# Performance work log

Hardware: AMD Instinct MI355X
Metric: run time of the kernel (lower is better)

Reference implementation:

```python
import jax, jax.numpy as jnp
import numpy as np

WEIGHT = 1000.0      # start/end cell penalty
LONELY_W = 15.0      # cell lit outside cluster
CLUSTER_W = 5.0      # cell unlit inside cluster
CELL_W = 20.0        # cell on a shortest manhattan path
CSIZE_W = 12.0       # cluster-size penalty
GAP_W = 300.0        # gap-to-endpoint penalty
H = W = 10


def _md(y1, x1, y2, x2):
    return jnp.abs(y1 - y2) + jnp.abs(x1 - x2)


def _per_sample(result, points):
    # result: [H, W] float, points: [2, 2] int (row, col) of start and end
    p0y, p0x = points[0, 0], points[0, 1]
    p1y, p1x = points[1, 0], points[1, 1]
    base = _md(p0y, p0x, p1y, p1x)

    loss_start = (2.0 - (result[p0y, p0x] + result[p1y, p1x])) * WEIGHT

    # 8-connected flood fill from start over cells whose value rounds to 1.
    mask = jnp.round(result) == 1.0
    seed = jnp.zeros((H, W), bool).at[p0y, p0x].set(True)

    def dilate(_, c):
        p = jnp.pad(c, 1)
        nb = (p[:-2, :-2] | p[:-2, 1:-1] | p[:-2, 2:] |
              p[1:-1, :-2] | p[1:-1, 2:] |
              p[2:, :-2] | p[2:, 1:-1] | p[2:, 2:])
        return c | (nb & mask)

    # 8-connected diameter of a 10x10 grid is 9; H+W iterations is a safe bound.
    cluster = jax.lax.fori_loop(0, H + W, dilate, seed)

    rows = jnp.arange(H)[:, None]
    cols = jnp.arange(W)[None, :]

    # per-cell manhattan detour penalty
    d2 = _md(rows, cols, p0y, p0x) + _md(rows, cols, p1y, p1x)
    delta = (d2 - base).astype(result.dtype)
    single_cell = jnp.sum(jnp.where(delta == 0.0,
                                    (1.0 - result) * CELL_W,
                                    result * delta * 0.5))

    # NB: the original tests [column, row] membership against [row, col]
    # cluster entries -> transposed membership map. Faithfully reproduced.
    in_cl = cluster.T
    csize = jnp.sum(cluster).astype(result.dtype)
    lonelyness = jnp.sum(jnp.where(in_cl, (1.0 - result) * CLUSTER_W,
                                   result * LONELY_W))
    cluster_size_pen = jnp.sum(jnp.where(in_cl, result * csize * CSIZE_W, 0.0))

    # nearest cluster cell to the end point (strict improvement over base)
    dist_end = _md(rows, cols, p1y, p1x)
    masked = jnp.where(cluster, dist_end, H * W + 10).reshape(-1)
    idx = jnp.argmin(masked)
    minval = masked[idx]
    better = minval < base
    ny = jnp.where(better, idx // W, p0y)
    nx = jnp.where(better, idx % W, p0x)
    gap = jnp.minimum(base, minval)

    oy = p1y - ny
    ox = p1x - nx

    def upd(cond, cy, cx, st):
        by, bx, bg = st
        d = _md(cy, cx, p1y, p1x)
        b = cond & (d < bg)
        return (jnp.where(b, cy, by), jnp.where(b, cx, bx), jnp.where(b, d, bg))

    st = (ny, nx, gap)
    c = ox < 0
    st = upd(c, ny, nx - 1, st)
    st = upd(c & (ny != 0), ny - 1, nx - 1, st)
    st = upd(c & (ny != H - 1), ny + 1, nx - 1, st)
    c = ox > 0
    st = upd(c, ny, nx + 1, st)
    st = upd(c & (ny != 0), ny - 1, nx + 1, st)
    st = upd(c & (ny != H - 1), ny + 1, nx + 1, st)
    st = upd(oy < 0, ny - 1, nx, st)
    st = upd(oy > 0, ny + 1, nx, st)
    ncy = jnp.clip(st[0], 0, H - 1)
    ncx = jnp.clip(st[1], 0, W - 1)

    gap_pen = gap.astype(result.dtype) * GAP_W * (1.0 - result[ncy, ncx])

    return loss_start + lonelyness + single_cell + cluster_size_pen + gap_pen


def setup_inputs() -> dict:
    key = jax.random.key(0)
    k1, k2 = jax.random.split(key)
    B = 262144
    result_given = jax.random.uniform(k1, (B, 1, H, W), dtype=jnp.float32)
    points_given = jax.random.randint(k2, (B, 2, 2), 0, 10, dtype=jnp.int64 if jax.config.jax_enable_x64 else jnp.int32)
    return {"result_given": result_given, "points_given": points_given}


def reference(result_given, points_given):
    losses = jax.vmap(_per_sample)(result_given[:, 0], points_given)
    return jnp.sum(losses).reshape(1)
```

## Files before the change

kernel.cpp:

```cpp
#include <hip/hip_runtime.h>
#include <cstdint>

#define GH 10
#define GW 10

__global__ __launch_bounds__(256, 1) void custom_loss_kernel(
    const float* __restrict__ result,
    const int* __restrict__ points,
    float* __restrict__ out,
    int B)
{
    const int t = blockIdx.x * blockDim.x + threadIdx.x;
    float loss = 0.f;
    if (t < B) {
        const float* __restrict__ r = result + (size_t)t * 100;
        const int4 p = ((const int4*)points)[t];
        const int p0y = p.x, p0x = p.y, p1y = p.z, p1x = p.w;
        const int dy0 = abs(p0y - p1y), dx0 = abs(p0x - p1x);
        const int base = dy0 + dx0;
        const int idx0 = p0y * GW + p0x;
        const int idx1 = p1y * GW + p1x;
        const float rs = r[idx0];
        const float re = r[idx1];

        float adxf[10], inboxf[10];
#pragma unroll
        for (int x = 0; x < 10; ++x) {
            const int a = abs(x - p0x) + abs(x - p1x) - dx0;
            adxf[x] = (float)a;
            inboxf[x] = (a == 0) ? 1.f : 0.f;
        }

        float sum_all = 0.f, sc = 0.f, boxSum = 0.f;
        uint64_t mlo = 0, mhi = 0;
#pragma unroll
        for (int y = 0; y < GH; ++y) {
            const float* rp = r + y * 10;
            const float4 a = *(const float4*)(rp);
            const float4 b = *(const float4*)(rp + 4);
            const float2 c = *(const float2*)(rp + 8);
            const float vv[10] = {a.x, a.y, a.z, a.w, b.x, b.y, b.z, b.w, c.x, c.y};
            const float rowacc = ((vv[0]+vv[1])+(vv[2]+vv[3])) +
                                 ((vv[4]+vv[5])+(vv[6]+vv[7])) + (vv[8]+vv[9]);
            sum_all += rowacc;
            const int ay = abs(y - p0y) + abs(y - p1y) - dy0;
            sc = fmaf((float)ay, rowacc, sc);
            float boxrow = 0.f;
            uint32_t rm = 0u;
#pragma unroll
            for (int x = 0; x < 10; ++x) {
                const float xv = vv[x];
                sc = fmaf(adxf[x], xv, sc);
                boxrow = fmaf(inboxf[x], xv, boxrow);
                rm |= (xv > 0.5f) ? (1u << x) : 0u;
            }
            boxSum += (ay == 0) ? boxrow : 0.f;
            if (y < 5) mlo |= (uint64_t)rm << (10 * y);
            else       mhi |= (uint64_t)rm << (10 * (y - 5));
        }

        const uint64_t M50 = (1ull << 50) - 1;
        const uint64_t C0  = 0x10040100401ull;
        const uint64_t NC0 = M50 & ~C0;
        const uint64_t NC9 = M50 & ~(C0 << 9);
        uint64_t clo = 0, chi = 0;
        if (idx0 < 50) clo = 1ull << idx0; else chi = 1ull << (idx0 - 50);
#pragma unroll 1
        for (int it = 0; it < GH + GW; ++it) {
            const uint64_t hlo = clo | ((clo << 1) & NC0) | ((clo >> 1) & NC9);
            const uint64_t hhi = chi | ((chi << 1) & NC0) | ((chi >> 1) & NC9);
            uint64_t nlo = (hlo | (hlo << 10) | (hlo >> 10) | ((hhi & 0x3FFull) << 40)) & mlo;
            uint64_t nhi = (hhi | (hhi << 10) | (hhi >> 10) | (hlo >> 40)) & mhi;
            nlo |= clo; nhi |= chi;
            if (nlo == clo && nhi == chi) break;
            clo = nlo; chi = nhi;
        }

        const int K = __popcll(clo) + __popcll(chi);

        float S_T = 0.f;
#pragma unroll
        for (int y = 0; y < GH; ++y) {
            const float* rp = r + y * 10;
            const float4 a = *(const float4*)(rp);
            const float4 b = *(const float4*)(rp + 4);
            const float2 c = *(const float2*)(rp + 8);
            const float vv[10] = {a.x, a.y, a.z, a.w, b.x, b.y, b.z, b.w, c.x, c.y};
#pragma unroll
            for (int x = 0; x < 10; ++x) {
                const int bpos = x * 10 + y;
                const uint32_t bit = (bpos < 50) ? (uint32_t)((clo >> bpos) & 1ull)
                                                 : (uint32_t)((chi >> (bpos - 50)) & 1ull);
                S_T = fmaf((float)bit, vv[x], S_T);
            }
        }

        int bestd = 1000, bidx = 0;
#pragma unroll
        for (int y = 0; y < GH; ++y) {
            const uint32_t rb = (uint32_t)((y < 5 ? (clo >> (10 * y))
                                                  : (chi >> (10 * (y - 5)))) & 0x3FFull);
            const uint32_t left  = rb & ((2u << p1x) - 1);
            const uint32_t right = rb >> p1x;
            const int dl = left  ? (p1x - (31 - __builtin_clz(left))) : 1000;
            const int dr = right ? __builtin_ctz(right) : 1000;
            int dx, xx;
            if (dl <= dr) { dx = dl; xx = p1x - dl; }
            else          { dx = dr; xx = p1x + dr; }
            const int d = abs(y - p1y) + dx;
            if (rb && d < bestd) { bestd = d; bidx = y * GW + xx; }
        }

        const bool better = bestd < base;
        const int ny = better ? bidx / 10 : p0y;
        const int nx = better ? bidx % 10 : p0x;
        const int gap = min(base, bestd);

        int by = ny, bx = nx, bg = gap;
        const int oy = p1y - ny, ox = p1x - nx;
        auto upd = [&](bool cond, int cy, int cx) {
            const int d = abs(cy - p1y) + abs(cx - p1x);
            if (cond && (d < bg)) { by = cy; bx = cx; bg = d; }
        };
        upd(ox < 0,                     ny,     nx - 1);
        upd((ox < 0) && (ny != 0),      ny - 1, nx - 1);
        upd((ox < 0) && (ny != GH - 1), ny + 1, nx - 1);
        upd(ox > 0,                     ny,     nx + 1);
        upd((ox > 0) && (ny != 0),      ny - 1, nx + 1);
        upd((ox > 0) && (ny != GH - 1), ny + 1, nx + 1);
        upd(oy < 0,                     ny - 1, nx);
        upd(oy > 0,                     ny + 1, nx);
        const int ncy = min(max(by, 0), GH - 1);
        const int ncx = min(max(bx, 0), GW - 1);
        const float rn = r[ncy * GW + ncx];

        const float csf = (float)K;
        const float nboxf = (float)((dy0 + 1) * (dx0 + 1));
        const float loss_start = (2.f - (rs + re)) * 1000.f;
        const float lon = 5.f * csf + 15.f * sum_all - 20.f * S_T;
        const float single_cell = 0.5f * sc + 20.f * (nboxf - boxSum);
        const float cpen = 12.f * csf * S_T;
        const float gap_pen = (float)gap * 300.f * (1.f - rn);
        loss = loss_start + lon + single_cell + cpen + gap_pen;
    }

#pragma unroll
    for (int off = 32; off > 0; off >>= 1)
        loss += __shfl_down(loss, off);
    __shared__ float wsum[4];
    const int lane = threadIdx.x & 63;
    const int wid = threadIdx.x >> 6;
    if (lane == 0) wsum[wid] = loss;
    __syncthreads();
    if (threadIdx.x == 0)
        atomicAdd(out, wsum[0] + wsum[1] + wsum[2] + wsum[3]);
}

extern "C" void kernel_launch(void* const* d_in, const int* in_sizes, int n_in,
                              void* d_out, int out_size, void* d_ws, size_t ws_size,
                              hipStream_t stream)
{
    const float* result = (const float*)d_in[0];
    const int* points   = (const int*)d_in[1];
    float* out = (float*)d_out;
    const int B = in_sizes[0] / 100;
    hipMemsetAsync(out, 0, sizeof(float), stream);
    const int block = 256;
    const int grid = (B + block - 1) / block;
    custom_loss_kernel<<<grid, block, 0, stream>>>(result, points, out, B);
}
```

Measured before the change: 182.6 us.

## Split each sample across two lanes, exchanging flood-fill halves via shuffles

Each sample is now handled by a pair of lanes, each owning five rows. Partial sums, the flood-fill bitmask halves and the nearest-cell search are combined with xor shuffles, and the launch bounds hint rises from 1 to 6 blocks. This doubles the thread count and cuts per-thread register use, aiming for more parallelism and better latency hiding on a memory-heavy kernel. The cost is a shuffle on every flood-fill iteration plus extra shuffles for the reductions, and the final scalar tail runs on only half the lanes.

```diff
diff --git a/kernel.cpp b/kernel.cpp
--- a/kernel.cpp
+++ b/kernel.cpp
@@ -4,17 +4,19 @@
 #define GH 10
 #define GW 10
 
-__global__ __launch_bounds__(256, 1) void custom_loss_kernel(
+__global__ __launch_bounds__(256, 6) void custom_loss_kernel(
     const float* __restrict__ result,
     const int* __restrict__ points,
     float* __restrict__ out,
     int B)
 {
-    const int t = blockIdx.x * blockDim.x + threadIdx.x;
+    const int tid = blockIdx.x * blockDim.x + threadIdx.x;
+    const int s = tid >> 1;
+    const int h = tid & 1;
     float loss = 0.f;
-    if (t < B) {
-        const float* __restrict__ r = result + (size_t)t * 100;
-        const int4 p = ((const int4*)points)[t];
+    if (s < B) {
+        const float* __restrict__ r = result + (size_t)s * 100;
+        const int4 p = ((const int4*)points)[s];
         const int p0y = p.x, p0x = p.y, p1y = p.z, p1x = p.w;
         const int dy0 = abs(p0y - p1y), dx0 = abs(p0x - p1x);
         const int base = dy0 + dx0;
@@ -23,83 +25,98 @@
         const float rs = r[idx0];
         const float re = r[idx1];
 
-        float adxf[10], inboxf[10];
+        float adxf[10];
+        uint32_t inbox_m = 0;
 #pragma unroll
         for (int x = 0; x < 10; ++x) {
             const int a = abs(x - p0x) + abs(x - p1x) - dx0;
             adxf[x] = (float)a;
-            inboxf[x] = (a == 0) ? 1.f : 0.f;
+            inbox_m |= (a == 0) ? (1u << x) : 0u;
         }
 
-        float sum_all = 0.f, sc = 0.f, boxSum = 0.f;
-        uint64_t mlo = 0, mhi = 0;
+        const int ybase = 5 * h;
+        const float* __restrict__ rh = r + ybase * 10;
+        float sum_h = 0.f, sc_h = 0.f, box_h = 0.f;
+        uint64_t mword = 0;
 #pragma unroll
-        for (int y = 0; y < GH; ++y) {
-            const float* rp = r + y * 10;
-            const float4 a = *(const float4*)(rp);
-            const float4 b = *(const float4*)(rp + 4);
-            const float2 c = *(const float2*)(rp + 8);
-            const float vv[10] = {a.x, a.y, a.z, a.w, b.x, b.y, b.z, b.w, c.x, c.y};
+        for (int i = 0; i < 5; ++i) {
+            const int y = ybase + i;
+            const float4 a4 = *(const float4*)(rh + i * 10);
+            const float4 b4 = *(const float4*)(rh + i * 10 + 4);
+            const float2 c2 = *(const float2*)(rh + i * 10 + 8);
+            const float vv[10] = {a4.x, a4.y, a4.z, a4.w,
+                                  b4.x, b4.y, b4.z, b4.w, c2.x, c2.y};
             const float rowacc = ((vv[0]+vv[1])+(vv[2]+vv[3])) +
                                  ((vv[4]+vv[5])+(vv[6]+vv[7])) + (vv[8]+vv[9]);
-            sum_all += rowacc;
+            sum_h += rowacc;
             const int ay = abs(y - p0y) + abs(y - p1y) - dy0;
-            sc = fmaf((float)ay, rowacc, sc);
+            sc_h = fmaf((float)ay, rowacc, sc_h);
             float boxrow = 0.f;
             uint32_t rm = 0u;
 #pragma unroll
             for (int x = 0; x < 10; ++x) {
                 const float xv = vv[x];
-                sc = fmaf(adxf[x], xv, sc);
-                boxrow = fmaf(inboxf[x], xv, boxrow);
+                sc_h = fmaf(adxf[x], xv, sc_h);
+                boxrow += ((inbox_m >> x) & 1u) ? xv : 0.f;
                 rm |= (xv > 0.5f) ? (1u << x) : 0u;
             }
-            boxSum += (ay == 0) ? boxrow : 0.f;
-            if (y < 5) mlo |= (uint64_t)rm << (10 * y);
-            else       mhi |= (uint64_t)rm << (10 * (y - 5));
+            box_h += (ay == 0) ? boxrow : 0.f;
+            mword |= (uint64_t)rm << (10 * i);
         }
+        const float sum_all = sum_h + __shfl_xor(sum_h, 1);
+        const float sc      = sc_h  + __shfl_xor(sc_h, 1);
+        const float boxSum  = box_h + __shfl_xor(box_h, 1);
 
         const uint64_t M50 = (1ull << 50) - 1;
         const uint64_t C0  = 0x10040100401ull;
         const uint64_t NC0 = M50 & ~C0;
         const uint64_t NC9 = M50 & ~(C0 << 9);
-        uint64_t clo = 0, chi = 0;
-        if (idx0 < 50) clo = 1ull << idx0; else chi = 1ull << (idx0 - 50);
+        uint64_t c = 0;
+        if (h == 0) { if (idx0 <  50) c = 1ull << idx0; }
+        else        { if (idx0 >= 50) c = 1ull << (idx0 - 50); }
 #pragma unroll 1
         for (int it = 0; it < GH + GW; ++it) {
-            const uint64_t hlo = clo | ((clo << 1) & NC0) | ((clo >> 1) & NC9);
-            const uint64_t hhi = chi | ((chi << 1) & NC0) | ((chi >> 1) & NC9);
-            uint64_t nlo = (hlo | (hlo << 10) | (hlo >> 10) | ((hhi & 0x3FFull) << 40)) & mlo;
-            uint64_t nhi = (hhi | (hhi << 10) | (hhi >> 10) | (hlo >> 40)) & mhi;
-            nlo |= clo; nhi |= chi;
-            if (nlo == clo && nhi == chi) break;
-            clo = nlo; chi = nhi;
+            const uint64_t ho = c | ((c << 1) & NC0) | ((c >> 1) & NC9);
+            const uint64_t hother =
+                (uint64_t)__shfl_xor((unsigned long long)ho, 1);
+            const uint64_t inc = h ? (hother >> 40) : ((hother & 0x3FFull) << 40);
+            const uint64_t n = ((ho | (ho << 10) | (ho >> 10) | inc) & mword) | c;
+            int ch = (n != c);
+            ch |= __shfl_xor(ch, 1);
+            c = n;
+            if (!ch) break;
         }
+        const int Kh = __popcll(c);
+        const int K = Kh + __shfl_xor(Kh, 1);
 
-        const int K = __popcll(clo) + __popcll(chi);
+        const uint64_t c_other = (uint64_t)__shfl_xor((unsigned long long)c, 1);
+        const uint64_t clo = h ? c_other : c;
+        const uint64_t chi = h ? c : c_other;
 
-        float S_T = 0.f;
+        const uint64_t wlo = clo >> (5 * h);
+        const uint64_t whi = chi >> (5 * h);
+        float st_h = 0.f;
 #pragma unroll
-        for (int y = 0; y < GH; ++y) {
-            const float* rp = r + y * 10;
-            const float4 a = *(const float4*)(rp);
-            const float4 b = *(const float4*)(rp + 4);
-            const float2 c = *(const float2*)(rp + 8);
-            const float vv[10] = {a.x, a.y, a.z, a.w, b.x, b.y, b.z, b.w, c.x, c.y};
+        for (int i = 0; i < 5; ++i) {
+            const float4 a4 = *(const float4*)(rh + i * 10);
+            const float4 b4 = *(const float4*)(rh + i * 10 + 4);
+            const float2 c2 = *(const float2*)(rh + i * 10 + 8);
+            const float vv[10] = {a4.x, a4.y, a4.z, a4.w,
+                                  b4.x, b4.y, b4.z, b4.w, c2.x, c2.y};
 #pragma unroll
             for (int x = 0; x < 10; ++x) {
-                const int bpos = x * 10 + y;
-                const uint32_t bit = (bpos < 50) ? (uint32_t)((clo >> bpos) & 1ull)
-                                                 : (uint32_t)((chi >> (bpos - 50)) & 1ull);
-                S_T = fmaf((float)bit, vv[x], S_T);
+                const uint64_t w = (x < 5) ? wlo : whi;
+                const uint32_t bit = (uint32_t)((w >> ((x % 5) * 10 + i)) & 1ull);
+                st_h = fmaf((float)bit, vv[x], st_h);
             }
         }
+        const float S_T = st_h + __shfl_xor(st_h, 1);
 
         int bestd = 1000, bidx = 0;
 #pragma unroll
-        for (int y = 0; y < GH; ++y) {
-            const uint32_t rb = (uint32_t)((y < 5 ? (clo >> (10 * y))
-                                                  : (chi >> (10 * (y - 5)))) & 0x3FFull);
+        for (int i = 0; i < 5; ++i) {
+            const int y = ybase + i;
+            const uint32_t rb = (uint32_t)((c >> (10 * i)) & 0x3FFull);
             const uint32_t left  = rb & ((2u << p1x) - 1);
             const uint32_t right = rb >> p1x;
             const int dl = left  ? (p1x - (31 - __builtin_clz(left))) : 1000;
@@ -110,38 +127,45 @@
             const int d = abs(y - p1y) + dx;
             if (rb && d < bestd) { bestd = d; bidx = y * GW + xx; }
         }
+        {
+            const int od = __shfl_xor(bestd, 1);
+            const int oi = __shfl_xor(bidx, 1);
+            if (od < bestd || (od == bestd && oi < bidx)) { bestd = od; bidx = oi; }
+        }
 
-        const bool better = bestd < base;
-        const int ny = better ? bidx / 10 : p0y;
-        const int nx = better ? bidx % 10 : p0x;
-        const int gap = min(base, bestd);
+        if (h == 0) {
+            const bool better = bestd < base;
+            const int ny = better ? bidx / 10 : p0y;
+            const int nx = better ? bidx % 10 : p0x;
+            const int gap = min(base, bestd);
 
-        int by = ny, bx = nx, bg = gap;
-        const int oy = p1y - ny, ox = p1x - nx;
-        auto upd = [&](bool cond, int cy, int cx) {
-            const int d = abs(cy - p1y) + abs(cx - p1x);
-            if (cond && (d < bg)) { by = cy; bx = cx; bg = d; }
-        };
-        upd(ox < 0,                     ny,     nx - 1);
-        upd((ox < 0) && (ny != 0),      ny - 1, nx - 1);
-        upd((ox < 0) && (ny != GH - 1), ny + 1, nx - 1);
-        upd(ox > 0,                     ny,     nx + 1);
-        upd((ox > 0) && (ny != 0),      ny - 1, nx + 1);
-        upd((ox > 0) && (ny != GH - 1), ny + 1, nx + 1);
-        upd(oy < 0,                     ny - 1, nx);
-        upd(oy > 0,                     ny + 1, nx);
-        const int ncy = min(max(by, 0), GH - 1);
-        const int ncx = min(max(bx, 0), GW - 1);
-        const float rn = r[ncy * GW + ncx];
+            int by = ny, bx = nx, bg = gap;
+            const int oy = p1y - ny, ox = p1x - nx;
+            auto upd = [&](bool cond, int cy, int cx) {
+                const int d = abs(cy - p1y) + abs(cx - p1x);
+                if (cond && (d < bg)) { by = cy; bx = cx; bg = d; }
+            };
+            upd(ox < 0,                     ny,     nx - 1);
+            upd((ox < 0) && (ny != 0),      ny - 1, nx - 1);
+            upd((ox < 0) && (ny != GH - 1), ny + 1, nx - 1);
+            upd(ox > 0,                     ny,     nx + 1);
+            upd((ox > 0) && (ny != 0),      ny - 1, nx + 1);
+            upd((ox > 0) && (ny != GH - 1), ny + 1, nx + 1);
+            upd(oy < 0,                     ny - 1, nx);
+            upd(oy > 0,                     ny + 1, nx);
+            const int ncy = min(max(by, 0), GH - 1);
+            const int ncx = min(max(bx, 0), GW - 1);
+            const float rn = r[ncy * GW + ncx];
 
-        const float csf = (float)K;
-        const float nboxf = (float)((dy0 + 1) * (dx0 + 1));
-        const float loss_start = (2.f - (rs + re)) * 1000.f;
-        const float lon = 5.f * csf + 15.f * sum_all - 20.f * S_T;
-        const float single_cell = 0.5f * sc + 20.f * (nboxf - boxSum);
-        const float cpen = 12.f * csf * S_T;
-        const float gap_pen = (float)gap * 300.f * (1.f - rn);
-        loss = loss_start + lon + single_cell + cpen + gap_pen;
+            const float csf = (float)K;
+            const float nboxf = (float)((dy0 + 1) * (dx0 + 1));
+            const float loss_start = (2.f - (rs + re)) * 1000.f;
+            const float lon = 5.f * csf + 15.f * sum_all - 20.f * S_T;
+            const float single_cell = 0.5f * sc + 20.f * (nboxf - boxSum);
+            const float cpen = 12.f * csf * S_T;
+            const float gap_pen = (float)gap * 300.f * (1.f - rn);
+            loss = loss_start + lon + single_cell + cpen + gap_pen;
+        }
     }
 
 #pragma unroll
@@ -166,6 +190,6 @@
     const int B = in_sizes[0] / 100;
     hipMemsetAsync(out, 0, sizeof(float), stream);
     const int block = 256;
-    const int grid = (B + block - 1) / block;
+    const int grid = (2 * B + block - 1) / block;
     custom_loss_kernel<<<grid, block, 0, stream>>>(result, points, out, B);
 }
```

After: 191.8 us. 5.0% more time.

## Split each sample across four lanes with coalesced float4 loads and shuffle reduction

Applied to the files above, without the earlier changes.

Each sample is now processed by four adjacent threads. Each thread loads interleaved float4 chunks, so accesses within a wave are coalesced, and computes partial sums and mask bits that are combined with xor shuffles. The flood fill and the endpoint search stay redundant across the four lanes. Launch bounds are raised to allow more waves per CU. This trades roughly four times the threads and duplicated serial flood-fill work for better memory coalescing and more latency hiding.

```diff
diff --git a/kernel.cpp b/kernel.cpp
--- a/kernel.cpp
+++ b/kernel.cpp
@@ -4,62 +4,70 @@
 #define GH 10
 #define GW 10
 
-__global__ __launch_bounds__(256, 1) void custom_loss_kernel(
+__global__ __launch_bounds__(256, 4) void custom_loss_kernel(
     const float* __restrict__ result,
     const int* __restrict__ points,
     float* __restrict__ out,
     int B)
 {
-    const int t = blockIdx.x * blockDim.x + threadIdx.x;
+    const int tid = blockIdx.x * blockDim.x + threadIdx.x;
+    const int s = tid >> 2;
+    const int q = tid & 3;
     float loss = 0.f;
-    if (t < B) {
-        const float* __restrict__ r = result + (size_t)t * 100;
-        const int4 p = ((const int4*)points)[t];
+    if (s < B) {
+        const float* __restrict__ r = result + (size_t)s * 100;
+        const int4 p = ((const int4*)points)[s];
         const int p0y = p.x, p0x = p.y, p1y = p.z, p1x = p.w;
         const int dy0 = abs(p0y - p1y), dx0 = abs(p0x - p1x);
-        const int base = dy0 + dx0;
+        const int base0 = dy0 + dx0;
         const int idx0 = p0y * GW + p0x;
         const int idx1 = p1y * GW + p1x;
         const float rs = r[idx0];
         const float re = r[idx1];
 
-        float adxf[10], inboxf[10];
+        float4 v4[7];
 #pragma unroll
-        for (int x = 0; x < 10; ++x) {
-            const int a = abs(x - p0x) + abs(x - p1x) - dx0;
-            adxf[x] = (float)a;
-            inboxf[x] = (a == 0) ? 1.f : 0.f;
-        }
+        for (int i = 0; i < 6; ++i) v4[i] = ((const float4*)r)[4 * i + q];
+        v4[6] = make_float4(0.f, 0.f, 0.f, 0.f);
+        if (q == 0) v4[6] = ((const float4*)r)[24];
 
-        float sum_all = 0.f, sc = 0.f, boxSum = 0.f;
+        const uint64_t M50 = (1ull << 50) - 1;
+        float sum_p = 0.f, sc_p = 0.f, box_p = 0.f;
         uint64_t mlo = 0, mhi = 0;
 #pragma unroll
-        for (int y = 0; y < GH; ++y) {
-            const float* rp = r + y * 10;
-            const float4 a = *(const float4*)(rp);
-            const float4 b = *(const float4*)(rp + 4);
-            const float2 c = *(const float2*)(rp + 8);
-            const float vv[10] = {a.x, a.y, a.z, a.w, b.x, b.y, b.z, b.w, c.x, c.y};
-            const float rowacc = ((vv[0]+vv[1])+(vv[2]+vv[3])) +
-                                 ((vv[4]+vv[5])+(vv[6]+vv[7])) + (vv[8]+vv[9]);
-            sum_all += rowacc;
-            const int ay = abs(y - p0y) + abs(y - p1y) - dy0;
-            sc = fmaf((float)ay, rowacc, sc);
-            float boxrow = 0.f;
-            uint32_t rm = 0u;
+        for (int i = 0; i < 7; ++i) {
+            const int kbase = (i < 6) ? 4 * (4 * i + q) : (96 + 4 * q);
+            const float vv[4] = {v4[i].x, v4[i].y, v4[i].z, v4[i].w};
+            uint32_t nib = 0;
 #pragma unroll
-            for (int x = 0; x < 10; ++x) {
-                const float xv = vv[x];
-                sc = fmaf(adxf[x], xv, sc);
-                boxrow = fmaf(inboxf[x], xv, boxrow);
-                rm |= (xv > 0.5f) ? (1u << x) : 0u;
+            for (int j = 0; j < 4; ++j) {
+                const int flat = kbase + j;
+                const int y = (flat * 205) >> 11;
+                const int x = flat - 10 * y;
+                const float v = vv[j];
+                sum_p += v;
+                const int af = abs(y - p0y) + abs(y - p1y) - dy0
+                             + abs(x - p0x) + abs(x - p1x) - dx0;
+                sc_p = fmaf((float)af, v, sc_p);
+                box_p += (af == 0) ? v : 0.f;
+                nib |= (v > 0.5f) ? (1u << j) : 0u;
             }
-            boxSum += (ay == 0) ? boxrow : 0.f;
-            if (y < 5) mlo |= (uint64_t)rm << (10 * y);
-            else       mhi |= (uint64_t)rm << (10 * (y - 5));
+            const uint64_t n64 = (uint64_t)nib;
+            const int shhi = (kbase >= 50) ? (kbase - 50) : 0;
+            mlo |= (kbase <= 44) ? (n64 << kbase)
+                                 : ((kbase == 48) ? ((n64 & 3ull) << 48) : 0);
+            mhi |= (kbase >= 52) ? (n64 << shhi)
+                                 : ((kbase == 48) ? (n64 >> 2) : 0);
         }
+        sum_p += __shfl_xor(sum_p, 1); sum_p += __shfl_xor(sum_p, 2);
+        sc_p  += __shfl_xor(sc_p, 1);  sc_p  += __shfl_xor(sc_p, 2);
+        box_p += __shfl_xor(box_p, 1); box_p += __shfl_xor(box_p, 2);
+        mlo |= (uint64_t)__shfl_xor((unsigned long long)mlo, 1);
+        mlo |= (uint64_t)__shfl_xor((unsigned long long)mlo, 2);
+        mhi |= (uint64_t)__shfl_xor((unsigned long long)mhi, 1);
+        mhi |= (uint64_t)__shfl_xor((unsigned long long)mhi, 2);
+        const float sum_all = sum_p, sc = sc_p, boxSum = box_p;
 
-        const uint64_t M50 = (1ull << 50) - 1;
         const uint64_t C0  = 0x10040100401ull;
         const uint64_t NC0 = M50 & ~C0;
         const uint64_t NC9 = M50 & ~(C0 << 9);
@@ -75,25 +83,26 @@
             if (nlo == clo && nhi == chi) break;
             clo = nlo; chi = nhi;
         }
-
         const int K = __popcll(clo) + __popcll(chi);
 
-        float S_T = 0.f;
+        float st_p = 0.f;
 #pragma unroll
-        for (int y = 0; y < GH; ++y) {
-            const float* rp = r + y * 10;
-            const float4 a = *(const float4*)(rp);
-            const float4 b = *(const float4*)(rp + 4);
-            const float2 c = *(const float2*)(rp + 8);
-            const float vv[10] = {a.x, a.y, a.z, a.w, b.x, b.y, b.z, b.w, c.x, c.y};
+        for (int i = 0; i < 7; ++i) {
+            const int kbase = (i < 6) ? 4 * (4 * i + q) : (96 + 4 * q);
+            const float vv[4] = {v4[i].x, v4[i].y, v4[i].z, v4[i].w};
 #pragma unroll
-            for (int x = 0; x < 10; ++x) {
-                const int bpos = x * 10 + y;
-                const uint32_t bit = (bpos < 50) ? (uint32_t)((clo >> bpos) & 1ull)
-                                                 : (uint32_t)((chi >> (bpos - 50)) & 1ull);
-                S_T = fmaf((float)bit, vv[x], S_T);
+            for (int j = 0; j < 4; ++j) {
+                const int flat = kbase + j;
+                const int y = (flat * 205) >> 11;
+                const int x = flat - 10 * y;
+                const int tr = x * 10 + y;
+                const int trs = (tr >= 50) ? (tr - 50) : tr;
+                const uint64_t w = (tr >= 50) ? chi : clo;
+                st_p = fmaf((float)((w >> trs) & 1ull), vv[j], st_p);
             }
         }
+        st_p += __shfl_xor(st_p, 1); st_p += __shfl_xor(st_p, 2);
+        const float S_T = st_p;
 
         int bestd = 1000, bidx = 0;
 #pragma unroll
@@ -111,10 +120,10 @@
             if (rb && d < bestd) { bestd = d; bidx = y * GW + xx; }
         }
 
-        const bool better = bestd < base;
+        const bool better = bestd < base0;
         const int ny = better ? bidx / 10 : p0y;
         const int nx = better ? bidx % 10 : p0x;
-        const int gap = min(base, bestd);
+        const int gap = min(base0, bestd);
 
         int by = ny, bx = nx, bg = gap;
         const int oy = p1y - ny, ox = p1x - nx;
@@ -142,6 +151,7 @@
         const float cpen = 12.f * csf * S_T;
         const float gap_pen = (float)gap * 300.f * (1.f - rn);
         loss = loss_start + lon + single_cell + cpen + gap_pen;
+        if (q != 0) loss = 0.f;
     }
 
 #pragma unroll
@@ -166,6 +176,6 @@
     const int B = in_sizes[0] / 100;
     hipMemsetAsync(out, 0, sizeof(float), stream);
     const int block = 256;
-    const int grid = (B + block - 1) / block;
+    const int grid = (4 * B + block - 1) / block;
     custom_loss_kernel<<<grid, block, 0, stream>>>(result, points, out, B);
 }
```

Measured after the change: 181.9 us. Within noise of the previous version (-0.4%).
